# Kernel optimization log

Hardware: AMD Instinct MI355X
Metric: run time of the kernel (lower is better)

The kernel has to match this reference:

```python
import jax, jax.numpy as jnp
import numpy as np

B, C, HGT, WID = 4096, 64, 8, 8
NUM_HEADS, HEAD_DIM = 8, 8
LN_EPS = 1e-5


def _make_chess_bias(size=8):
    idx = np.arange(size * size)
    r, c = idx // size, idx % size
    dr = np.abs(r[:, None] - r[None, :])
    dc = np.abs(c[:, None] - c[None, :])
    dist = dr + dc
    diag = dr == dc
    bias = np.where(dist == 0, 0.1, np.where(dist <= 2, 0.05, np.where(diag, 0.03, 0.0)))
    return jnp.asarray(bias, dtype=jnp.float32)


def setup_inputs() -> dict:
    key = jax.random.key(0)
    k = jax.random.split(key, 4)
    E = C
    return {
        "x": jax.random.normal(k[0], (B, C, HGT, WID), dtype=jnp.float32),
        "pos_embed": jax.random.normal(k[1], (1, C, HGT, WID), dtype=jnp.float32),
        "ln_gamma": jnp.ones((E,), dtype=jnp.float32),
        "ln_beta": jnp.zeros((E,), dtype=jnp.float32),
        "qkv_w": jax.random.normal(k[2], (3 * E, E), dtype=jnp.float32) / np.sqrt(E),
        "qkv_b": jnp.zeros((3 * E,), dtype=jnp.float32),
        "out_w": jax.random.normal(k[3], (E, E), dtype=jnp.float32) / np.sqrt(E),
        "out_b": jnp.zeros((E,), dtype=jnp.float32),
        "chess_bias": _make_chess_bias(8),
        "stage": 1,
    }


def reference(x, pos_embed, ln_gamma, ln_beta, qkv_w, qkv_b, out_w, out_b, chess_bias, stage):
    # stage is fixed (=1); params above are the stage-1 params.
    x = x + pos_embed                                   # [B, C, H, W]
    b, c, h, w = x.shape
    x_flat = x.reshape(b, c, h * w).transpose(0, 2, 1)  # [B, S, E], S = H*W
    # LayerNorm over embed dim
    mu = jnp.mean(x_flat, axis=-1, keepdims=True)
    var = jnp.var(x_flat, axis=-1, keepdims=True)
    x_norm = (x_flat - mu) * jax.lax.rsqrt(var + LN_EPS) * ln_gamma + ln_beta
    # QKV projection (torch Linear: y = x W^T + b)
    qkv = x_norm @ qkv_w.T + qkv_b                      # [B, S, 3E]
    s = h * w
    qkv = qkv.reshape(b, s, 3, NUM_HEADS, HEAD_DIM)
    q = qkv[:, :, 0].transpose(0, 2, 1, 3)              # [B, H, S, D]
    k = qkv[:, :, 1].transpose(0, 2, 1, 3)
    v = qkv[:, :, 2].transpose(0, 2, 1, 3)
    scores = jnp.einsum("bhsd,bhtd->bhst", q, k) * (HEAD_DIM ** -0.5)
    scores = scores + chess_bias[None, None, :, :]
    attn = jax.nn.softmax(scores, axis=-1)              # dropout = identity (eval)
    out = jnp.einsum("bhst,bhtd->bhsd", attn, v)        # [B, H, S, D]
    out = out.transpose(0, 2, 1, 3).reshape(b, s, c)    # [B, S, E]
    attn_out = out @ out_w.T + out_b
    x_out = x_flat + attn_out                           # residual
    return x_out.transpose(0, 2, 1).reshape(b, c, h, w)
```

## Files before the change

kernel.cpp:

```cpp
#include <hip/hip_runtime.h>
#include <stdint.h>


typedef __attribute__((ext_vector_type(8))) __bf16 bfrag;
typedef __attribute__((ext_vector_type(4))) __bf16 bf4;
typedef __attribute__((ext_vector_type(4))) float f32x4;

#define MFMA16(a, b, c) __builtin_amdgcn_mfma_f32_16x16x32_bf16((a), (b), (c), 0, 0, 0)

static __device__ __forceinline__ bfrag bsplat(float v) {
  bfrag z;
#pragma unroll
  for (int i = 0; i < 8; i++) z[i] = (__bf16)v;
  return z;
}

static __device__ __forceinline__ bfrag cvt8(const float* __restrict__ p) {
  float4 a = *(const float4*)p, b = *(const float4*)(p + 4);
  bfrag r;
  r[0] = (__bf16)a.x; r[1] = (__bf16)a.y; r[2] = (__bf16)a.z; r[3] = (__bf16)a.w;
  r[4] = (__bf16)b.x; r[5] = (__bf16)b.y; r[6] = (__bf16)b.z; r[7] = (__bf16)b.w;
  return r;
}

__global__ __launch_bounds__(256, 3) void chess_attn_kernel(
    const float* __restrict__ xg,    const float* __restrict__ posg,
    const float* __restrict__ gam,   const float* __restrict__ bet,
    const float* __restrict__ qkvw,  const float* __restrict__ qkvb,
    const float* __restrict__ outw,  const float* __restrict__ outb,
    const float* __restrict__ biasg, float* __restrict__ outg) {
  __shared__ __attribute__((aligned(16))) __bf16 P1[2][64 * 136];
  __shared__ __attribute__((aligned(16))) __bf16 P2[2][64 * 72];

  const int tid = threadIdx.x, lane = tid & 63, w = tid >> 6;
  const int m = lane & 15, g = lane >> 4;
  const int b0 = blockIdx.x * 2;
  const float LN2I = 1.4426950408889634f;
  const float SCL2 = 0.35355339059327373f * 1.4426950408889634f;

  {
    const float4* pp = (const float4*)(posg + (size_t)lane * 64 + w * 16);
    float4 pv[4] = {pp[0], pp[1], pp[2], pp[3]};
#pragma unroll
    for (int it = 0; it < 2; it++) {
      float* XP = (float*)P1[it];
      const float4* px = (const float4*)(xg + ((size_t)(b0 + it) * 64 + lane) * 64 + w * 16);
#pragma unroll
      for (int v = 0; v < 4; v++) {
        float4 xv = px[v];
        const int s = w * 16 + v * 4;
        XP[(s + 0) * 68 + lane] = xv.x + pv[v].x;
        XP[(s + 1) * 68 + lane] = xv.y + pv[v].y;
        XP[(s + 2) * 68 + lane] = xv.z + pv[v].z;
        XP[(s + 3) * 68 + lane] = xv.w + pv[v].w;
      }
    }
  }

  {
    const int s = tid >> 2, q = tid & 3;
    const float4* pg = (const float4*)(gam + q * 16);
    const float4* pb = (const float4*)(bet + q * 16);
    float4 g0 = pg[0], g1 = pg[1], g2 = pg[2], g3 = pg[3];
    float4 b0v = pb[0], b1 = pb[1], b2 = pb[2], b3 = pb[3];
    float gr[16] = {g0.x, g0.y, g0.z, g0.w, g1.x, g1.y, g1.z, g1.w,
                    g2.x, g2.y, g2.z, g2.w, g3.x, g3.y, g3.z, g3.w};
    float br[16] = {b0v.x, b0v.y, b0v.z, b0v.w, b1.x, b1.y, b1.z, b1.w,
                    b2.x, b2.y, b2.z, b2.w, b3.x, b3.y, b3.z, b3.w};
#pragma unroll
    for (int it = 0; it < 2; it++) {
      const float* XP = (const float*)P1[it];
      const float4* pr = (const float4*)&XP[s * 68 + q * 16];
      float4 x0 = pr[0], x1 = pr[1], x2 = pr[2], x3 = pr[3];
      float xr[16] = {x0.x, x0.y, x0.z, x0.w, x1.x, x1.y, x1.z, x1.w,
                      x2.x, x2.y, x2.z, x2.w, x3.x, x3.y, x3.z, x3.w};
      float sum = 0.f, ss = 0.f;
#pragma unroll
      for (int i = 0; i < 16; i++) { sum += xr[i]; ss = fmaf(xr[i], xr[i], ss); }
      sum += __shfl_xor(sum, 1); ss += __shfl_xor(ss, 1);
      sum += __shfl_xor(sum, 2); ss += __shfl_xor(ss, 2);
      const float mu = sum * 0.015625f;
      const float rs = __builtin_amdgcn_rsqf(ss * 0.015625f - mu * mu + 1e-5f);
      bfrag o0, o1;
#pragma unroll
      for (int i = 0; i < 8; i++) o0[i] = (__bf16)((xr[i] - mu) * rs * gr[i] + br[i]);
#pragma unroll
      for (int i = 0; i < 8; i++) o1[i] = (__bf16)((xr[8 + i] - mu) * rs * gr[8 + i] + br[8 + i]);
      *(bfrag*)&P2[it][s * 72 + q * 16] = o0;
      *(bfrag*)&P2[it][s * 72 + q * 16 + 8] = o1;
    }
  }
  __syncthreads();

  bfrag XF[2][4][2];
#pragma unroll
  for (int it = 0; it < 2; it++)
#pragma unroll
    for (int st = 0; st < 4; st++) {
      XF[it][st][0] = *(const bfrag*)&P2[it][(st * 16 + m) * 72 + g * 8];
      XF[it][st][1] = *(const bfrag*)&P2[it][(st * 16 + m) * 72 + 32 + g * 8];
    }
  __syncthreads();

  {
#pragma unroll
    for (int i = 0; i < 2; i++) {
      const int nt = w + 4 * i;
      bfrag AW0 = cvt8(qkvw + (size_t)(nt * 16 + m) * 64 + g * 8);
      bfrag AW1 = cvt8(qkvw + (size_t)(nt * 16 + m) * 64 + 32 + g * 8);
      float4 qb4 = *(const float4*)(qkvb + nt * 16 + g * 4);
      const float qs = (i == 0) ? SCL2 : 1.0f;
      const float qbx = qb4.x * qs, qby = qb4.y * qs;
      const float qbz = qb4.z * qs, qbw = qb4.w * qs;
#pragma unroll
      for (int it = 0; it < 2; it++)
#pragma unroll
        for (int st = 0; st < 4; st++) {
          f32x4 c = {0.f, 0.f, 0.f, 0.f};
          c = MFMA16(AW0, XF[it][st][0], c);
          c = MFMA16(AW1, XF[it][st][1], c);
          bf4 pk;
          pk[0] = (__bf16)fmaf(c[0], qs, qbx); pk[1] = (__bf16)fmaf(c[1], qs, qby);
          pk[2] = (__bf16)fmaf(c[2], qs, qbz); pk[3] = (__bf16)fmaf(c[3], qs, qbw);
          *(bf4*)&P1[it][(st * 16 + m) * 136 + nt * 16 + g * 4] = pk;
        }
    }
    {
      const int n = 128 + w * 16 + m;
      bfrag BV0 = cvt8(qkvw + (size_t)n * 64 + g * 8);
      bfrag BV1 = cvt8(qkvw + (size_t)n * 64 + 32 + g * 8);
      const float vb = qkvb[n];
#pragma unroll
      for (int it = 0; it < 2; it++)
#pragma unroll
        for (int st = 0; st < 4; st++) {
          f32x4 c = {0.f, 0.f, 0.f, 0.f};
          c = MFMA16(XF[it][st][0], BV0, c);
          c = MFMA16(XF[it][st][1], BV1, c);
          bf4 pk;
#pragma unroll
          for (int r = 0; r < 4; r++) pk[r] = (__bf16)(c[r] + vb);
          *(bf4*)&P2[it][(w * 16 + m) * 72 + st * 16 + g * 4] = pk;
        }
    }
  }

  const bfrag ZF  = bsplat(0.f);
  const bfrag ONE = bsplat(1.f);
  __bf16* PS = &P2[0][0];
  const int a7 = m & 7;
  const int rowoff0 = (16 * w + a7) * 72 + (m >> 3) * 4608;
  const int rowoff1 = rowoff0 + 8 * 72;
  const int rot = 8 * a7;

  bfrag VA[2][2][2];
#pragma unroll
  for (int it = 0; it < 2; it++)
#pragma unroll
    for (int hl = 0; hl < 2; hl++)
#pragma unroll
      for (int kf = 0; kf < 2; kf++)
        VA[it][hl][kf] = (m < 8)
            ? *(const bfrag*)&P2[it][(16 * w + 8 * hl + m) * 72 + kf * 32 + g * 8]
            : ((m == 8) ? ONE : ZF);

  __builtin_amdgcn_s_setprio(1);
#pragma unroll 2
  for (int st = 0; st < 4; st++) {
    f32x4 binit[4];
#pragma unroll
    for (int tt = 0; tt < 4; tt++) {
      float4 bv = *(const float4*)(biasg + (size_t)(st * 16 + m) * 64 + tt * 16 + g * 4);
      binit[tt][0] = bv.x * LN2I; binit[tt][1] = bv.y * LN2I;
      binit[tt][2] = bv.z * LN2I; binit[tt][3] = bv.w * LN2I;
    }
#pragma unroll
    for (int hl = 0; hl < 2; hl++) {
      const int h8 = 16 * w + 8 * hl;
      const int rowoff = hl ? rowoff1 : rowoff0;
#pragma unroll
      for (int it = 0; it < 2; it++) {
        const __bf16* Pit = P1[it];
        bfrag QB = (lane < 16) ? *(const bfrag*)&Pit[(st * 16 + m) * 136 + h8] : ZF;
        f32x4 sc[4];
#pragma unroll
        for (int tt = 0; tt < 4; tt++) {
          bfrag KA = (lane < 16) ? *(const bfrag*)&Pit[(tt * 16 + m) * 136 + 64 + h8] : ZF;
          sc[tt] = MFMA16(KA, QB, binit[tt]);
        }
#pragma unroll
        for (int tt = 0; tt < 4; tt++) {
          bf4 pr;
          pr[0] = (__bf16)__builtin_amdgcn_exp2f(sc[tt][0]);
          pr[1] = (__bf16)__builtin_amdgcn_exp2f(sc[tt][1]);
          pr[2] = (__bf16)__builtin_amdgcn_exp2f(sc[tt][2]);
          pr[3] = (__bf16)__builtin_amdgcn_exp2f(sc[tt][3]);
          *(bf4*)&PS[rowoff + ((tt * 16 + g * 4 + rot) & 63)] = pr;
        }
        bfrag PB0 = *(const bfrag*)&PS[rowoff + ((g * 8 + rot) & 63)];
        bfrag PB1 = *(const bfrag*)&PS[rowoff + ((32 + g * 8 + rot) & 63)];
        f32x4 oo = {0.f, 0.f, 0.f, 0.f};
        oo = MFMA16(VA[it][hl][0], PB0, oo);
        oo = MFMA16(VA[it][hl][1], PB1, oo);
        const float rsum = __builtin_amdgcn_rcpf(__shfl(oo[0], 32 + m));
        bf4 ov;
#pragma unroll
        for (int r = 0; r < 4; r++) ov[r] = (__bf16)(oo[r] * rsum);
        if (g < 2) *(bf4*)&P1[it][(st * 16 + m) * 136 + h8 + g * 4] = ov;
      }
    }
  }
  __builtin_amdgcn_s_setprio(0);
  __syncthreads();

  {
    bfrag A0[2], A1[2];
#pragma unroll
    for (int it = 0; it < 2; it++) {
      A0[it] = *(const bfrag*)&P1[it][(w * 16 + m) * 136 + g * 8];
      A1[it] = *(const bfrag*)&P1[it][(w * 16 + m) * 136 + 32 + g * 8];
    }
    const int sbase = w * 16 + g * 4;
#pragma unroll
    for (int et = 0; et < 4; et++) {
      const int e = et * 16 + m;
      bfrag BW0 = cvt8(outw + (size_t)e * 64 + g * 8);
      bfrag BW1 = cvt8(outw + (size_t)e * 64 + 32 + g * 8);
      const float ob = outb[e];
      float4 pv = *(const float4*)(posg + (size_t)e * 64 + sbase);
#pragma unroll
      for (int it = 0; it < 2; it++) {
        const size_t xoff = (size_t)(b0 + it) * 4096;
        f32x4 c = {0.f, 0.f, 0.f, 0.f};
        c = MFMA16(A0[it], BW0, c);
        c = MFMA16(A1[it], BW1, c);
        float4 xv = *(const float4*)(xg + xoff + (size_t)e * 64 + sbase);
        float4 o;
        o.x = c[0] + ob + xv.x + pv.x;
        o.y = c[1] + ob + xv.y + pv.y;
        o.z = c[2] + ob + xv.z + pv.z;
        o.w = c[3] + ob + xv.w + pv.w;
        *(float4*)(outg + xoff + (size_t)e * 64 + sbase) = o;
      }
    }
  }
}

extern "C" void kernel_launch(void* const* d_in, const int* in_sizes, int n_in,
                              void* d_out, int out_size, void* d_ws, size_t ws_size,
                              hipStream_t stream) {
  const float* xg   = (const float*)d_in[0];
  const float* pos  = (const float*)d_in[1];
  const float* gam  = (const float*)d_in[2];
  const float* bet  = (const float*)d_in[3];
  const float* qkvw = (const float*)d_in[4];
  const float* qkvb = (const float*)d_in[5];
  const float* outw = (const float*)d_in[6];
  const float* outb = (const float*)d_in[7];
  const float* cb   = (const float*)d_in[8];
  float* out = (float*)d_out;
  const int B = in_sizes[0] / (64 * 64);
  hipLaunchKernelGGL(chess_attn_kernel, dim3(B / 2), dim3(256), 0, stream,
                     xg, pos, gam, bet, qkvw, qkvb, outw, outb, cb, out);
}
```

Measured before the change: 191.7 us.

## Hoist K fragments per head, prefetch residual x, drop LDS swizzle and setprio

The attention loop is reordered so the head-half loop is outermost. K fragments for both batch items are loaded into registers once per head-half instead of once per query tile, and the normalized attention output is written back into the K slot rather than the Q slot. The residual x tile is prefetched into registers before the attention phase so its global-load latency overlaps compute. The rotation swizzle on the probability scratch writes and the s_setprio hints are removed, which saves address arithmetic but may bring back LDS bank conflicts and adds register pressure.

```diff
diff --git a/kernel.cpp b/kernel.cpp
--- a/kernel.cpp
+++ b/kernel.cpp
@@ -145,13 +145,24 @@
     }
   }
 
+  float4 xf4[2][4];
+  {
+    const int sbase = w * 16 + g * 4;
+#pragma unroll
+    for (int et = 0; et < 4; et++) {
+      const int e = et * 16 + m;
+#pragma unroll
+      for (int it = 0; it < 2; it++)
+        xf4[it][et] = *(const float4*)(xg + (size_t)(b0 + it) * 4096 + (size_t)e * 64 + sbase);
+    }
+  }
+
   const bfrag ZF  = bsplat(0.f);
   const bfrag ONE = bsplat(1.f);
   __bf16* PS = &P2[0][0];
   const int a7 = m & 7;
-  const int rowoff0 = (16 * w + a7) * 72 + (m >> 3) * 4608;
-  const int rowoff1 = rowoff0 + 8 * 72;
-  const int rot = 8 * a7;
+  const int rowoffA = (16 * w + a7) * 72 + (m >> 3) * 4608;
+  const int rowoffB = rowoffA + 8 * 72;
 
   bfrag VA[2][2][2];
 #pragma unroll
@@ -164,30 +175,32 @@
             ? *(const bfrag*)&P2[it][(16 * w + 8 * hl + m) * 72 + kf * 32 + g * 8]
             : ((m == 8) ? ONE : ZF);
 
-  __builtin_amdgcn_s_setprio(1);
-#pragma unroll 2
-  for (int st = 0; st < 4; st++) {
-    f32x4 binit[4];
-#pragma unroll
-    for (int tt = 0; tt < 4; tt++) {
-      float4 bv = *(const float4*)(biasg + (size_t)(st * 16 + m) * 64 + tt * 16 + g * 4);
-      binit[tt][0] = bv.x * LN2I; binit[tt][1] = bv.y * LN2I;
-      binit[tt][2] = bv.z * LN2I; binit[tt][3] = bv.w * LN2I;
-    }
-#pragma unroll
-    for (int hl = 0; hl < 2; hl++) {
-      const int h8 = 16 * w + 8 * hl;
-      const int rowoff = hl ? rowoff1 : rowoff0;
+#pragma unroll
+  for (int hl = 0; hl < 2; hl++) {
+    const int h8 = 16 * w + 8 * hl;
+    bfrag KA[2][4];
+#pragma unroll
+    for (int it = 0; it < 2; it++)
+#pragma unroll
+      for (int tt = 0; tt < 4; tt++)
+        KA[it][tt] = (lane < 16) ? *(const bfrag*)&P1[it][(tt * 16 + m) * 136 + 64 + h8] : ZF;
+#pragma unroll
+    for (int st = 0; st < 4; st++) {
+      f32x4 binit[4];
+#pragma unroll
+      for (int tt = 0; tt < 4; tt++) {
+        float4 bv = *(const float4*)(biasg + (size_t)(st * 16 + m) * 64 + tt * 16 + g * 4);
+        binit[tt][0] = bv.x * LN2I; binit[tt][1] = bv.y * LN2I;
+        binit[tt][2] = bv.z * LN2I; binit[tt][3] = bv.w * LN2I;
+      }
 #pragma unroll
       for (int it = 0; it < 2; it++) {
-        const __bf16* Pit = P1[it];
-        bfrag QB = (lane < 16) ? *(const bfrag*)&Pit[(st * 16 + m) * 136 + h8] : ZF;
+        const int rowoff = it ? rowoffB : rowoffA;
+        bfrag QB = (lane < 16) ? *(const bfrag*)&P1[it][(st * 16 + m) * 136 + h8] : ZF;
         f32x4 sc[4];
 #pragma unroll
-        for (int tt = 0; tt < 4; tt++) {
-          bfrag KA = (lane < 16) ? *(const bfrag*)&Pit[(tt * 16 + m) * 136 + 64 + h8] : ZF;
-          sc[tt] = MFMA16(KA, QB, binit[tt]);
-        }
+        for (int tt = 0; tt < 4; tt++)
+          sc[tt] = MFMA16(KA[it][tt], QB, binit[tt]);
 #pragma unroll
         for (int tt = 0; tt < 4; tt++) {
           bf4 pr;
@@ -195,10 +208,10 @@
           pr[1] = (__bf16)__builtin_amdgcn_exp2f(sc[tt][1]);
           pr[2] = (__bf16)__builtin_amdgcn_exp2f(sc[tt][2]);
           pr[3] = (__bf16)__builtin_amdgcn_exp2f(sc[tt][3]);
-          *(bf4*)&PS[rowoff + ((tt * 16 + g * 4 + rot) & 63)] = pr;
+          *(bf4*)&PS[rowoff + tt * 16 + g * 4] = pr;
         }
-        bfrag PB0 = *(const bfrag*)&PS[rowoff + ((g * 8 + rot) & 63)];
-        bfrag PB1 = *(const bfrag*)&PS[rowoff + ((32 + g * 8 + rot) & 63)];
+        bfrag PB0 = *(const bfrag*)&PS[rowoff + g * 8];
+        bfrag PB1 = *(const bfrag*)&PS[rowoff + 32 + g * 8];
         f32x4 oo = {0.f, 0.f, 0.f, 0.f};
         oo = MFMA16(VA[it][hl][0], PB0, oo);
         oo = MFMA16(VA[it][hl][1], PB1, oo);
@@ -206,19 +219,18 @@
         bf4 ov;
 #pragma unroll
         for (int r = 0; r < 4; r++) ov[r] = (__bf16)(oo[r] * rsum);
-        if (g < 2) *(bf4*)&P1[it][(st * 16 + m) * 136 + h8 + g * 4] = ov;
-      }
-    }
-  }
-  __builtin_amdgcn_s_setprio(0);
+        if (g < 2) *(bf4*)&P1[it][(st * 16 + m) * 136 + 64 + h8 + g * 4] = ov;
+      }
+    }
+  }
   __syncthreads();
 
   {
     bfrag A0[2], A1[2];
 #pragma unroll
     for (int it = 0; it < 2; it++) {
-      A0[it] = *(const bfrag*)&P1[it][(w * 16 + m) * 136 + g * 8];
-      A1[it] = *(const bfrag*)&P1[it][(w * 16 + m) * 136 + 32 + g * 8];
+      A0[it] = *(const bfrag*)&P1[it][(w * 16 + m) * 136 + 64 + g * 8];
+      A1[it] = *(const bfrag*)&P1[it][(w * 16 + m) * 136 + 96 + g * 8];
     }
     const int sbase = w * 16 + g * 4;
 #pragma unroll
@@ -234,7 +246,7 @@
         f32x4 c = {0.f, 0.f, 0.f, 0.f};
         c = MFMA16(A0[it], BW0, c);
         c = MFMA16(A1[it], BW1, c);
-        float4 xv = *(const float4*)(xg + xoff + (size_t)e * 64 + sbase);
+        float4 xv = xf4[it][et];
         float4 o;
         o.x = c[0] + ob + xv.x + pv.x;
         o.y = c[1] + ob + xv.y + pv.y;
```

New measurement: 207.0 us. +8.0%, slower.
